# Optimization experiments

Measured on AMD Instinct MI355X. Metric: run time of the kernel, lower is better.

## Reference

```python
import jax, jax.numpy as jnp
import numpy as np

EPS = 1e-5
NEG_SLOPE = 0.01  # torch LeakyReLU default

def setup_inputs() -> dict:
    N, D, T, H = 4096, 64, 60, 128
    key = jax.random.key(0)
    ks = jax.random.split(key, 12)
    s_ih = 1.0 / np.sqrt(H)
    return {
        "x": jax.random.normal(ks[0], (N, D, T), dtype=jnp.float32),
        "bn1_gamma": jnp.ones((D,), jnp.float32),
        "bn1_beta": jnp.zeros((D,), jnp.float32),
        "W_ih": jax.random.uniform(ks[1], (4 * H, D), jnp.float32, -s_ih, s_ih),
        "W_hh": jax.random.uniform(ks[2], (4 * H, H), jnp.float32, -s_ih, s_ih),
        "b_ih": jax.random.uniform(ks[3], (4 * H,), jnp.float32, -s_ih, s_ih),
        "b_hh": jax.random.uniform(ks[4], (4 * H,), jnp.float32, -s_ih, s_ih),
        "bn2_gamma": jnp.ones((H,), jnp.float32),
        "bn2_beta": jnp.zeros((H,), jnp.float32),
        "W_t": jax.random.uniform(ks[5], (H, H), jnp.float32, -s_ih, s_ih),
        "b_t": jax.random.uniform(ks[6], (H,), jnp.float32, -s_ih, s_ih),
        "a": jax.random.normal(ks[7], (2 * H, 1), dtype=jnp.float32),
        "W_fc": jax.random.uniform(ks[8], (H, H), jnp.float32, -s_ih, s_ih),
        "b_fc": jax.random.uniform(ks[9], (H,), jnp.float32, -s_ih, s_ih),
        "W_out": jax.random.uniform(ks[10], (1, H), jnp.float32, -s_ih, s_ih),
        "b_out": jax.random.uniform(ks[11], (1,), jnp.float32, -s_ih, s_ih),
    }

def _leaky(z):
    return jnp.where(z >= 0, z, NEG_SLOPE * z)

def _lstm_last(x, W_ih, W_hh, b_ih, b_hh):
    # x: [N, T, D] -> last hidden state [N, H]
    N, T, D = x.shape
    H = W_hh.shape[1]
    # precompute input contributions for all timesteps: [T, N, 4H]
    xg = jnp.einsum('ntd,gd->tng', x, W_ih) + b_ih + b_hh
    h0 = jnp.zeros((N, H), x.dtype)
    c0 = jnp.zeros((N, H), x.dtype)
    def step(carry, g):
        h, c = carry
        gates = g + h @ W_hh.T
        i, f, gg, o = jnp.split(gates, 4, axis=-1)
        i = jax.nn.sigmoid(i)
        f = jax.nn.sigmoid(f)
        gg = jnp.tanh(gg)
        o = jax.nn.sigmoid(o)
        c = f * c + i * gg
        h = o * jnp.tanh(c)
        return (h, c), None
    (h, _), _ = jax.lax.scan(step, (h0, c0), xg)
    return h

def reference(x, bn1_gamma, bn1_beta, W_ih, W_hh, b_ih, b_hh,
              bn2_gamma, bn2_beta, W_t, b_t, a, W_fc, b_fc, W_out, b_out):
    # BatchNorm1d over channels of [N, D, T] (training-mode batch stats)
    m1 = x.mean(axis=(0, 2), keepdims=True)
    v1 = x.var(axis=(0, 2), keepdims=True)
    xn = (x - m1) * jax.lax.rsqrt(v1 + EPS)
    xn = xn * bn1_gamma[None, :, None] + bn1_beta[None, :, None]
    xs = jnp.transpose(xn, (0, 2, 1))  # [N, T, D]
    hidden = _lstm_last(xs, W_ih, W_hh, b_ih, b_hh)  # [N, H]
    # BatchNorm1d on [N, H]
    m2 = hidden.mean(axis=0, keepdims=True)
    v2 = hidden.var(axis=0, keepdims=True)
    hidden = (hidden - m2) * jax.lax.rsqrt(v2 + EPS) * bn2_gamma + bn2_beta
    # attention: scores[i,j] = a1.t[j] + a2.t[i]  (decomposed, no NxNx2H concat)
    H = hidden.shape[1]
    t = hidden @ W_t.T + b_t  # [N, H]
    s1 = t @ a[:H, 0]   # contribution of column node j
    s2 = t @ a[H:, 0]   # contribution of row node i
    scores = _leaky(s2[:, None] + s1[None, :])  # [N, N]
    att = jax.nn.softmax(scores, axis=1)
    h2 = att @ hidden + hidden
    h3 = _leaky(h2 @ W_fc.T + b_fc)
    out = jax.nn.sigmoid(h3 @ W_out.T + b_out)  # [N, 1]
    return out.squeeze(-1)
```

## Files before the change

### kernel.cpp

```cpp
#include <hip/hip_runtime.h>
#include <math.h>

constexpr int NN = 4096, DD = 64, TT = 60, HH = 128, GG = 512, KK = 192;

typedef _Float16 h8 __attribute__((ext_vector_type(8)));
typedef float f4 __attribute__((ext_vector_type(4)));

constexpr size_t XNT = 0;
constexpr size_t WFRG = (size_t)TT * NN * DD / 2;
constexpr size_t BSUM = WFRG + 98304 / 2;
constexpr size_t SC1 = BSUM + GG;
constexpr size_t SH1 = SC1 + DD;
constexpr size_t HID = SH1 + DD;
constexpr size_t HBN = HID + (size_t)NN * HH;
constexpr size_t SC2 = HBN + (size_t)NN * HH;
constexpr size_t SH2 = SC2 + HH;
constexpr size_t U1O = SH2 + HH;
constexpr size_t U2O = U1O + HH;
constexpr size_t CCO = U2O + HH;
constexpr size_t S1O = CCO + 4;
constexpr size_t S2O = S1O + NN;
constexpr size_t H2O = S2O + NN;
constexpr size_t SSUM = H2O + (size_t)NN * HH;
constexpr size_t SC16 = SSUM + 392;

__device__ __forceinline__ float fastrcp_(float x) { return __builtin_amdgcn_rcpf(x); }
__device__ __forceinline__ float sigmoidf_(float x) { return fastrcp_(1.f + __expf(-x)); }
__device__ __forceinline__ float tanhfast_(float x) { return 1.f - 2.f * fastrcp_(__expf(2.f * x) + 1.f); }
__device__ __forceinline__ float leakyf_(float z) { return fmaxf(z, 0.01f * z); }

__device__ __forceinline__ unsigned fenc_(float f) {
    unsigned b = __float_as_uint(f);
    return (b & 0x80000000u) ? ~b : (b | 0x80000000u);
}
__device__ __forceinline__ float fdec_(unsigned u) {
    return (u & 0x80000000u) ? __uint_as_float(u & 0x7fffffffu) : __uint_as_float(~u);
}

constexpr int TSTR = 264;

__global__ __launch_bounds__(256) void k_pre(const float* __restrict__ x,
                                             const float* __restrict__ Wih,
                                             const float* __restrict__ Whh,
                                             const float* __restrict__ Wt,
                                             const float* __restrict__ bt,
                                             const float* __restrict__ a,
                                             float* __restrict__ ws) {
    int b = blockIdx.x;
    int tid = threadIdx.x;
    if (b >= 1024) {
        if (b == 1408) {
            int k = tid;
            if (k < HH) {
                float u1 = 0.f, u2 = 0.f;
                for (int j = 0; j < HH; j++) {
                    float w = Wt[j * HH + k];
                    u1 = fmaf(w, a[j], u1);
                    u2 = fmaf(w, a[HH + j], u2);
                }
                ws[U1O + k] = u1;
                ws[U2O + k] = u2;
                if (k == 0) {
                    float c1 = 0.f, c2 = 0.f;
                    for (int j = 0; j < HH; j++) {
                        c1 = fmaf(bt[j], a[j], c1);
                        c2 = fmaf(bt[j], a[HH + j], c2);
                    }
                    ws[CCO] = c1;
                    ws[CCO + 1] = c2;
                    ((unsigned*)ws)[CCO + 2] = fenc_(-1e30f);
                }
            }
            return;
        }
        int o = (b - 1024) * 256 + tid;
        _Float16* wf = (_Float16*)(ws + WFRG);
        int j = o & 7;
        int lane = (o >> 3) & 63;
        int rest = o >> 9;
        int ks = rest % 6;
        int gw = rest / 6;
        int g = gw & 3, w = gw >> 2;
        int col = g * 128 + w * 16 + (lane & 15);
        int k = ks * 32 + (lane >> 4) * 8 + j;
        float v = (k < DD) ? Wih[col * DD + k] : Whh[col * HH + (k - DD)];
        wf[o] = (_Float16)v;
        return;
    }
    __shared__ _Float16 stg[TT * TSTR];
    __shared__ float rs[256], rss[256];
    const float4* xb = (const float4*)(x + (size_t)b * 15360);
#pragma unroll
    for (int q = 0; q < 15; q++) {
        int f = q * 256 + tid;
        float4 v = xb[f];
        int k = f / 15, t0 = (f - k * 15) * 4;
        stg[(t0 + 0) * TSTR + k] = (_Float16)v.x;
        stg[(t0 + 1) * TSTR + k] = (_Float16)v.y;
        stg[(t0 + 2) * TSTR + k] = (_Float16)v.z;
        stg[(t0 + 3) * TSTR + k] = (_Float16)v.w;
    }
    __syncthreads();
    {
        int k = tid;
        float s = 0.f, ss = 0.f;
#pragma unroll
        for (int t = 0; t < TT; t++) {
            float v = (float)stg[t * TSTR + k];
            s += v;
            ss = fmaf(v, v, ss);
        }
        rs[tid] = s; rss[tid] = ss;
    }
    __syncthreads();
    if (tid < 64) {
        float ts = rs[tid] + rs[64 + tid] + rs[128 + tid] + rs[192 + tid];
        float tss = rss[tid] + rss[64 + tid] + rss[128 + tid] + rss[192 + tid];
        float* pp = ws + H2O + (size_t)b * 128;
        pp[tid] = ts;
        pp[64 + tid] = tss;
    }
    _Float16* outp = (_Float16*)ws;
    int n0 = b * 4;
    for (int p = tid; p < 3840; p += 256) {
        int t = p >> 6, i = p & 63;
        *(uint2*)(outp + ((size_t)t * NN + n0) * DD + i * 4) =
            *(const uint2*)(stg + t * TSTR + i * 4);
    }
}

__global__ __launch_bounds__(256) void k_fin1(const float* __restrict__ g1,
                                              const float* __restrict__ b1,
                                              const float* __restrict__ Wih,
                                              const float* __restrict__ bih,
                                              const float* __restrict__ bhh,
                                              float* __restrict__ ws) {
    __shared__ float p2[8][128];
    __shared__ float scs[64], shs[64];
    int tid = threadIdx.x;
    for (int i = tid; i < 392; i += 256) ws[SSUM + i] = 0.f;
    {
        int rb = tid >> 5;
        int c0 = (tid & 31) * 4;
        const float* pb = ws + H2O + (size_t)rb * 128 * 128;
        float4 s4 = {0.f, 0.f, 0.f, 0.f};
        for (int bb = 0; bb < 128; bb++) {
            float4 v = *(const float4*)(pb + (size_t)bb * 128 + c0);
            s4.x += v.x; s4.y += v.y; s4.z += v.z; s4.w += v.w;
        }
        p2[rb][c0 + 0] = s4.x;
        p2[rb][c0 + 1] = s4.y;
        p2[rb][c0 + 2] = s4.z;
        p2[rb][c0 + 3] = s4.w;
    }
    __syncthreads();
    if (tid < 64) {
        float s_ = 0.f, ss_ = 0.f;
#pragma unroll
        for (int g = 0; g < 8; g++) {
            s_ += p2[g][tid];
            ss_ += p2[g][64 + tid];
        }
        float cnt = (float)(NN * TT);
        float m = s_ / cnt;
        float var = ss_ / cnt - m * m;
        float sc = g1[tid] * rsqrtf(var + 1e-5f);
        scs[tid] = sc;
        shs[tid] = b1[tid] - m * sc;
        ((_Float16*)(ws + SC16))[tid] = (_Float16)sc;
    }
    __syncthreads();
    for (int c = tid; c < GG; c += 256) {
        float bsum = bih[c] + bhh[c];
        const float4* wr = (const float4*)(Wih + c * 64);
#pragma unroll
        for (int q = 0; q < 16; q++) {
            float4 wv = wr[q];
            bsum = fmaf(wv.x, shs[q * 4], fmaf(wv.y, shs[q * 4 + 1],
                   fmaf(wv.z, shs[q * 4 + 2], fmaf(wv.w, shs[q * 4 + 3], bsum))));
        }
        ws[BSUM + c] = bsum;
    }
}

__global__ __launch_bounds__(512, 1) void k_lstm(float* __restrict__ ws) {
    int tid = threadIdx.x;
    int w = tid >> 6, lane = tid & 63;
    int quad = lane >> 4, m = lane & 15;
    int r0 = blockIdx.x * 16;
    __shared__ _Float16 hlds[2][16][136];
    const _Float16* wf = (const _Float16*)(ws + WFRG);

    h8 bw[4][6];
#pragma unroll
    for (int g = 0; g < 4; g++)
#pragma unroll
        for (int ks = 0; ks < 6; ks++)
            bw[g][ks] = *(const h8*)(wf + ((((w * 4 + g) * 6 + ks) * 64 + lane) * 8));

    f4 xbias[4];
#pragma unroll
    for (int g = 0; g < 4; g++) {
        float bv = ws[BSUM + g * 128 + w * 16 + m];
        xbias[g] = (f4){bv, bv, bv, bv};
    }

    const _Float16* sc16 = (const _Float16*)(ws + SC16);
    {
        h8 scv0 = *(const h8*)(sc16 + quad * 8);
        h8 scv1 = *(const h8*)(sc16 + 32 + quad * 8);
#pragma unroll
        for (int g = 0; g < 4; g++) { bw[g][0] *= scv0; bw[g][1] *= scv1; }
    }

    for (int p = tid; p < 2 * 16 * 136; p += 512) ((_Float16*)hlds)[p] = (_Float16)0.f;

    f4 cst = {};
    float hv[4];
    const _Float16* xb = (const _Float16*)ws + (size_t)(r0 + m) * DD + quad * 8;
    int col = w * 16 + m;
    __syncthreads();

    h8 ax0 = *(const h8*)xb;
    h8 ax1 = *(const h8*)(xb + 32);
    f4 xA[4], xB[4];
#pragma unroll
    for (int g = 0; g < 4; g++) xA[g] = __builtin_amdgcn_mfma_f32_16x16x32_f16(ax0, bw[g][0], xbias[g], 0, 0, 0);
#pragma unroll
    for (int g = 0; g < 4; g++) xA[g] = __builtin_amdgcn_mfma_f32_16x16x32_f16(ax1, bw[g][1], xA[g], 0, 0, 0);

    for (int t = 0; t < TT; t += 2) {
        {
            h8 ah[4];
            const _Float16* hb = &hlds[1][m][quad * 8];
#pragma unroll
            for (int ks = 0; ks < 4; ks++) ah[ks] = *(const h8*)(hb + ks * 32);
            const _Float16* xp = xb + (size_t)(t + 1) * NN * DD;
            h8 nx0 = *(const h8*)xp;
            h8 nx1 = *(const h8*)(xp + 32);
#pragma unroll
            for (int ks = 0; ks < 4; ks++)
#pragma unroll
                for (int g = 0; g < 4; g++)
                    xA[g] = __builtin_amdgcn_mfma_f32_16x16x32_f16(ah[ks], bw[g][ks + 2], xA[g], 0, 0, 0);
#pragma unroll
            for (int r = 0; r < 4; r++) {
                float ig = sigmoidf_(xA[0][r]);
                float fg = sigmoidf_(xA[1][r]);
                float gg = tanhfast_(xA[2][r]);
                float og = sigmoidf_(xA[3][r]);
                float c = fmaf(fg, cst[r], ig * gg);
                cst[r] = c;
                hv[r] = og * tanhfast_(c);
            }
            _Float16* wbuf = &hlds[0][0][0];
#pragma unroll
            for (int r = 0; r < 4; r++) wbuf[(quad * 4 + r) * 136 + col] = (_Float16)hv[r];
#pragma unroll
            for (int g = 0; g < 4; g++) xB[g] = __builtin_amdgcn_mfma_f32_16x16x32_f16(nx0, bw[g][0], xbias[g], 0, 0, 0);
#pragma unroll
            for (int g = 0; g < 4; g++) xB[g] = __builtin_amdgcn_mfma_f32_16x16x32_f16(nx1, bw[g][1], xB[g], 0, 0, 0);
            asm volatile("s_waitcnt lgkmcnt(0)\n\ts_barrier" ::: "memory");
        }
        {
            h8 ah[4];
            const _Float16* hb = &hlds[0][m][quad * 8];
#pragma unroll
            for (int ks = 0; ks < 4; ks++) ah[ks] = *(const h8*)(hb + ks * 32);
            h8 nx0 = {}, nx1 = {};
            if (t + 2 < TT) {
                const _Float16* xp = xb + (size_t)(t + 2) * NN * DD;
                nx0 = *(const h8*)xp;
                nx1 = *(const h8*)(xp + 32);
            }
#pragma unroll
            for (int ks = 0; ks < 4; ks++)
#pragma unroll
                for (int g = 0; g < 4; g++)
                    xB[g] = __builtin_amdgcn_mfma_f32_16x16x32_f16(ah[ks], bw[g][ks + 2], xB[g], 0, 0, 0);
#pragma unroll
            for (int r = 0; r < 4; r++) {
                float ig = sigmoidf_(xB[0][r]);
                float fg = sigmoidf_(xB[1][r]);
                float gg = tanhfast_(xB[2][r]);
                float og = sigmoidf_(xB[3][r]);
                float c = fmaf(fg, cst[r], ig * gg);
                cst[r] = c;
                hv[r] = og * tanhfast_(c);
            }
            _Float16* wbuf = &hlds[1][0][0];
#pragma unroll
            for (int r = 0; r < 4; r++) wbuf[(quad * 4 + r) * 136 + col] = (_Float16)hv[r];
#pragma unroll
            for (int g = 0; g < 4; g++) xA[g] = __builtin_amdgcn_mfma_f32_16x16x32_f16(nx0, bw[g][0], xbias[g], 0, 0, 0);
#pragma unroll
            for (int g = 0; g < 4; g++) xA[g] = __builtin_amdgcn_mfma_f32_16x16x32_f16(nx1, bw[g][1], xA[g], 0, 0, 0);
            asm volatile("s_waitcnt lgkmcnt(0)\n\ts_barrier" ::: "memory");
        }
    }
#pragma unroll
    for (int r = 0; r < 4; r++)
        ws[HID + (size_t)(r0 + quad * 4 + r) * HH + col] = hv[r];

    float s = hv[0] + hv[1] + hv[2] + hv[3];
    float ss = fmaf(hv[0], hv[0], fmaf(hv[1], hv[1], fmaf(hv[2], hv[2], hv[3] * hv[3])));
    s += __shfl_xor(s, 16, 64); s += __shfl_xor(s, 32, 64);
    ss += __shfl_xor(ss, 16, 64); ss += __shfl_xor(ss, 32, 64);
    if (quad == 0) {
        atomicAdd(&ws[SSUM + 132 + col], s);
        atomicAdd(&ws[SSUM + 260 + col], ss);
    }
}

__global__ void k_hbn(const float* __restrict__ g2,
                      const float* __restrict__ b2,
                      float* __restrict__ ws) {
    __shared__ float sc[HH], sh[HH], u1s[HH], u2s[HH];
    __shared__ _Float16 swz[4096];
    int tid = threadIdx.x;
    if (tid < HH) {
        float mm = ws[SSUM + 132 + tid] * (1.f / (float)NN);
        float var = ws[SSUM + 260 + tid] * (1.f / (float)NN) - mm * mm;
        float scv = g2[tid] * rsqrtf(var + 1e-5f);
        sc[tid] = scv;
        sh[tid] = b2[tid] - mm * scv;
        u1s[tid] = ws[U1O + tid]; u2s[tid] = ws[U2O + tid];
    }
    __syncthreads();
    int r = tid >> 3, l = tid & 7;
    int n = blockIdx.x * 32 + r;
    const float* hr = ws + HID + (size_t)n * HH;
    float* hb = ws + HBN + (size_t)n * HH;
    int lanehi = (r >> 3);
    int jj = r & 7;
    float d1 = 0.f, d2 = 0.f;
    int k0 = l * 16;
#pragma unroll
    for (int q4 = 0; q4 < 4; q4++) {
        float4 hv4 = *(const float4*)&hr[k0 + q4 * 4];
        float4 o;
#pragma unroll
        for (int c = 0; c < 4; c++) {
            int kk = k0 + q4 * 4 + c;
            float v = fmaf(((const float*)&hv4)[c], sc[kk], sh[kk]);
            ((float*)&o)[c] = v;
            swz[l * 512 + (lanehi * 16 + (kk & 15)) * 8 + jj] = (_Float16)v;
            d1 = fmaf(v, u1s[kk], d1);
            d2 = fmaf(v, u2s[kk], d2);
        }
        *(float4*)&hb[k0 + q4 * 4] = o;
    }
#pragma unroll
    for (int o = 1; o < 8; o <<= 1) { d1 += __shfl_xor(d1, o, 64); d2 += __shfl_xor(d2, o, 64); }
    if (l == 0) {
        float s1 = d1 + ws[CCO];
        ws[S1O + n] = s1;
        ws[S2O + n] = d2 + ws[CCO + 1];
        atomicMax((unsigned*)ws + CCO + 2, fenc_(s1));
    }
    __syncthreads();
    _Float16* dst = (_Float16*)ws + (size_t)blockIdx.x * 4096;
    for (int p = tid; p < 512; p += 256)
        *(h8*)(dst + p * 8) = *(const h8*)(swz + p * 8);
}

__global__ __launch_bounds__(512, 1) void k_attfc(const float* __restrict__ Wfc,
                                                  const float* __restrict__ bfc,
                                                  const float* __restrict__ Wout,
                                                  const float* __restrict__ bout,
                                                  float* __restrict__ ws,
                                                  float* __restrict__ out) {
    __shared__ float ls1[NN];
    __shared__ float red[4][16][132];
    __shared__ float psr[4][16];
    __shared__ float h2s[16][132];
    int tid = threadIdx.x;
    int w = tid >> 6, lane = tid & 63;
    int quad = lane >> 4, m = lane & 15;
    int whalf = w >> 2, jsplit = w & 3;
    int n0 = blockIdx.x * 16;
    for (int i = tid; i < NN; i += 512) ls1[i] = ws[S1O + i];
    __syncthreads();
    float s1max = fdec_(((unsigned*)ws)[CCO + 2]);
    float s2n = ws[S2O + n0 + m];
    float mi = leakyf_(s2n + s1max);
    const _Float16* hbsw = (const _Float16*)ws;
    f4 acc[4] = {};
    float psum = 0.f;
    for (int jt0 = 0; jt0 < 32; jt0++) {
        int jt = jsplit * 32 + jt0;
        const float* sp = &ls1[jt * 32 + quad * 8];
        h8 ap;
        float ps = 0.f;
#pragma unroll
        for (int jj = 0; jj < 8; jj++) {
            float z = s2n + sp[jj];
            float p = __expf(leakyf_(z) - mi);
            ps += p;
            ap[jj] = (_Float16)p;
        }
        psum += ps;
#pragma unroll
        for (int hgi = 0; hgi < 4; hgi++) {
            int hg = whalf * 4 + hgi;
            h8 bb = *(const h8*)(hbsw + ((size_t)(jt * 8 + hg) * 64 + lane) * 8);
            acc[hgi] = __builtin_amdgcn_mfma_f32_16x16x32_f16(ap, bb, acc[hgi], 0, 0, 0);
        }
    }
    psum += __shfl_xor(psum, 16, 64);
    psum += __shfl_xor(psum, 32, 64);
    if (whalf == 0 && lane < 16) psr[jsplit][lane] = psum;
#pragma unroll
    for (int hgi = 0; hgi < 4; hgi++) {
        int h = (whalf * 4 + hgi) * 16 + m;
#pragma unroll
        for (int r = 0; r < 4; r++)
            red[jsplit][quad * 4 + r][h] = acc[hgi][r];
    }
    __syncthreads();
    if (tid < 16) {
        float pt = psr[0][tid] + psr[1][tid] + psr[2][tid] + psr[3][tid];
        psr[0][tid] = fastrcp_(pt);
    }
    __syncthreads();
#pragma unroll
    for (int cc = 0; cc < 4; cc++) {
        int c = cc * 512 + tid;
        int row = c >> 7, h = c & 127;
        float v = red[0][row][h] + red[1][row][h] + red[2][row][h] + red[3][row][h];
        h2s[row][h] = fmaf(v, psr[0][row], ws[HBN + (size_t)(n0 + row) * HH + h]);
    }
    __syncthreads();
    int row = tid >> 5, jj = tid & 31;
    float po = 0.f;
#pragma unroll
    for (int q = 0; q < 4; q++) {
        int j = q * 32 + jj;
        const float4* wr = (const float4*)(Wfc + (size_t)j * HH);
        float a = 0.f;
#pragma unroll 8
        for (int kq = 0; kq < 32; kq++) {
            float4 wv = wr[kq];
            float4 hv = *(const float4*)&h2s[row][kq * 4];
            a = fmaf(wv.x, hv.x, fmaf(wv.y, hv.y, fmaf(wv.z, hv.z, fmaf(wv.w, hv.w, a))));
        }
        po = fmaf(leakyf_(a + bfc[j]), Wout[j], po);
    }
#pragma unroll
    for (int o = 1; o < 32; o <<= 1) po += __shfl_xor(po, o, 64);
    if (jj == 0) out[n0 + row] = fastrcp_(1.f + __expf(-(po + bout[0])));
}

extern "C" void kernel_launch(void* const* d_in, const int* in_sizes, int n_in,
                              void* d_out, int out_size, void* d_ws, size_t ws_size,
                              hipStream_t stream) {
    const float* x = (const float*)d_in[0];
    const float* bn1_g = (const float*)d_in[1];
    const float* bn1_b = (const float*)d_in[2];
    const float* W_ih = (const float*)d_in[3];
    const float* W_hh = (const float*)d_in[4];
    const float* b_ih = (const float*)d_in[5];
    const float* b_hh = (const float*)d_in[6];
    const float* bn2_g = (const float*)d_in[7];
    const float* bn2_b = (const float*)d_in[8];
    const float* W_t = (const float*)d_in[9];
    const float* b_t = (const float*)d_in[10];
    const float* a = (const float*)d_in[11];
    const float* W_fc = (const float*)d_in[12];
    const float* b_fc = (const float*)d_in[13];
    const float* W_out = (const float*)d_in[14];
    const float* b_out = (const float*)d_in[15];
    float* ws = (float*)d_ws;
    float* out = (float*)d_out;

    k_pre<<<1409, 256, 0, stream>>>(x, W_ih, W_hh, W_t, b_t, a, ws);
    k_fin1<<<1, 256, 0, stream>>>(bn1_g, bn1_b, W_ih, b_ih, b_hh, ws);
    k_lstm<<<NN / 16, 512, 0, stream>>>(ws);
    k_hbn<<<NN / 32, 256, 0, stream>>>(bn2_g, bn2_b, ws);
    k_attfc<<<NN / 16, 512, 0, stream>>>(W_fc, b_fc, W_out, b_out, ws, out);
}
```

Before: 265.4 us.

## Widen small kernels, pad staging stride, double-buffer attention MFMA loop

The single-block BN1 finalize kernel now runs with 1024 threads, which shortens each thread's serial reduction over the partial sums. The hidden-BN kernel uses 512 threads, each handling 8 features instead of 16. In the attention kernel the loop is software-pipelined: the next tile's B fragments are loaded and its probabilities computed before the current tile's MFMAs issue. The k_pre LDS staging stride changes from 264 to 266 to avoid bank conflicts. Together these aim to cut serial latency in the small kernels and hide load latency in attention, at the cost of higher register pressure.

Measured after the change: 284.3 us. 1.07x slower.

```diff
diff --git a/kernel.cpp b/kernel.cpp
--- a/kernel.cpp
+++ b/kernel.cpp
@@ -37,7 +37,7 @@
     return (u & 0x80000000u) ? __uint_as_float(u & 0x7fffffffu) : __uint_as_float(~u);
 }
 
-constexpr int TSTR = 264;
+constexpr int TSTR = 266;
 
 __global__ __launch_bounds__(256) void k_pre(const float* __restrict__ x,
                                              const float* __restrict__ Wih,
@@ -129,22 +129,22 @@
     }
 }
 
-__global__ __launch_bounds__(256) void k_fin1(const float* __restrict__ g1,
-                                              const float* __restrict__ b1,
-                                              const float* __restrict__ Wih,
-                                              const float* __restrict__ bih,
-                                              const float* __restrict__ bhh,
-                                              float* __restrict__ ws) {
-    __shared__ float p2[8][128];
+__global__ __launch_bounds__(1024) void k_fin1(const float* __restrict__ g1,
+                                               const float* __restrict__ b1,
+                                               const float* __restrict__ Wih,
+                                               const float* __restrict__ bih,
+                                               const float* __restrict__ bhh,
+                                               float* __restrict__ ws) {
+    __shared__ float p2[32][128];
     __shared__ float scs[64], shs[64];
     int tid = threadIdx.x;
-    for (int i = tid; i < 392; i += 256) ws[SSUM + i] = 0.f;
+    if (tid < 392) ws[SSUM + tid] = 0.f;
     {
         int rb = tid >> 5;
         int c0 = (tid & 31) * 4;
-        const float* pb = ws + H2O + (size_t)rb * 128 * 128;
+        const float* pb = ws + H2O + (size_t)rb * 32 * 128;
         float4 s4 = {0.f, 0.f, 0.f, 0.f};
-        for (int bb = 0; bb < 128; bb++) {
+        for (int bb = 0; bb < 32; bb++) {
             float4 v = *(const float4*)(pb + (size_t)bb * 128 + c0);
             s4.x += v.x; s4.y += v.y; s4.z += v.z; s4.w += v.w;
         }
@@ -157,7 +157,7 @@
     if (tid < 64) {
         float s_ = 0.f, ss_ = 0.f;
 #pragma unroll
-        for (int g = 0; g < 8; g++) {
+        for (int g = 0; g < 32; g++) {
             s_ += p2[g][tid];
             ss_ += p2[g][64 + tid];
         }
@@ -170,14 +170,18 @@
         ((_Float16*)(ws + SC16))[tid] = (_Float16)sc;
     }
     __syncthreads();
-    for (int c = tid; c < GG; c += 256) {
+    if (tid < GG) {
+        int c = tid;
         float bsum = bih[c] + bhh[c];
         const float4* wr = (const float4*)(Wih + c * 64);
+        float4 sh4[16];
+#pragma unroll
+        for (int q = 0; q < 16; q++) sh4[q] = *(const float4*)&shs[q * 4];
 #pragma unroll
         for (int q = 0; q < 16; q++) {
             float4 wv = wr[q];
-            bsum = fmaf(wv.x, shs[q * 4], fmaf(wv.y, shs[q * 4 + 1],
-                   fmaf(wv.z, shs[q * 4 + 2], fmaf(wv.w, shs[q * 4 + 3], bsum))));
+            bsum = fmaf(wv.x, sh4[q].x, fmaf(wv.y, sh4[q].y,
+                   fmaf(wv.z, sh4[q].z, fmaf(wv.w, sh4[q].w, bsum))));
         }
         ws[BSUM + c] = bsum;
     }
@@ -312,9 +316,9 @@
     }
 }
 
-__global__ void k_hbn(const float* __restrict__ g2,
-                      const float* __restrict__ b2,
-                      float* __restrict__ ws) {
+__global__ __launch_bounds__(512) void k_hbn(const float* __restrict__ g2,
+                                             const float* __restrict__ b2,
+                                             float* __restrict__ ws) {
     __shared__ float sc[HH], sh[HH], u1s[HH], u2s[HH];
     __shared__ _Float16 swz[4096];
     int tid = threadIdx.x;
@@ -327,16 +331,14 @@
         u1s[tid] = ws[U1O + tid]; u2s[tid] = ws[U2O + tid];
     }
     __syncthreads();
-    int r = tid >> 3, l = tid & 7;
+    int r = tid >> 4, l = tid & 15;
     int n = blockIdx.x * 32 + r;
     const float* hr = ws + HID + (size_t)n * HH;
     float* hb = ws + HBN + (size_t)n * HH;
-    int lanehi = (r >> 3);
-    int jj = r & 7;
     float d1 = 0.f, d2 = 0.f;
-    int k0 = l * 16;
-#pragma unroll
-    for (int q4 = 0; q4 < 4; q4++) {
+    int k0 = l * 8;
+#pragma unroll
+    for (int q4 = 0; q4 < 2; q4++) {
         float4 hv4 = *(const float4*)&hr[k0 + q4 * 4];
         float4 o;
 #pragma unroll
@@ -344,14 +346,14 @@
             int kk = k0 + q4 * 4 + c;
             float v = fmaf(((const float*)&hv4)[c], sc[kk], sh[kk]);
             ((float*)&o)[c] = v;
-            swz[l * 512 + (lanehi * 16 + (kk & 15)) * 8 + jj] = (_Float16)v;
+            swz[(kk >> 4) * 512 + ((r >> 3) * 16 + (kk & 15)) * 8 + (r & 7)] = (_Float16)v;
             d1 = fmaf(v, u1s[kk], d1);
             d2 = fmaf(v, u2s[kk], d2);
         }
         *(float4*)&hb[k0 + q4 * 4] = o;
     }
 #pragma unroll
-    for (int o = 1; o < 8; o <<= 1) { d1 += __shfl_xor(d1, o, 64); d2 += __shfl_xor(d2, o, 64); }
+    for (int o = 1; o < 16; o <<= 1) { d1 += __shfl_xor(d1, o, 64); d2 += __shfl_xor(d2, o, 64); }
     if (l == 0) {
         float s1 = d1 + ws[CCO];
         ws[S1O + n] = s1;
@@ -360,8 +362,7 @@
     }
     __syncthreads();
     _Float16* dst = (_Float16*)ws + (size_t)blockIdx.x * 4096;
-    for (int p = tid; p < 512; p += 256)
-        *(h8*)(dst + p * 8) = *(const h8*)(swz + p * 8);
+    *(h8*)(dst + tid * 8) = *(const h8*)(swz + tid * 8);
 }
 
 __global__ __launch_bounds__(512, 1) void k_attfc(const float* __restrict__ Wfc,
@@ -387,26 +388,51 @@
     const _Float16* hbsw = (const _Float16*)ws;
     f4 acc[4] = {};
     float psum = 0.f;
-    for (int jt0 = 0; jt0 < 32; jt0++) {
-        int jt = jsplit * 32 + jt0;
-        const float* sp = &ls1[jt * 32 + quad * 8];
-        h8 ap;
-        float ps = 0.f;
-#pragma unroll
-        for (int jj = 0; jj < 8; jj++) {
-            float z = s2n + sp[jj];
-            float p = __expf(leakyf_(z) - mi);
-            ps += p;
-            ap[jj] = (_Float16)p;
-        }
-        psum += ps;
-#pragma unroll
-        for (int hgi = 0; hgi < 4; hgi++) {
-            int hg = whalf * 4 + hgi;
-            h8 bb = *(const h8*)(hbsw + ((size_t)(jt * 8 + hg) * 64 + lane) * 8);
-            acc[hgi] = __builtin_amdgcn_mfma_f32_16x16x32_f16(ap, bb, acc[hgi], 0, 0, 0);
-        }
-    }
+
+#define AP_COMPUTE(JT, APV, PSV)                                        \
+    {                                                                   \
+        const float* sp_ = &ls1[(JT) * 32 + quad * 8];                  \
+        PSV = 0.f;                                                      \
+        _Pragma("unroll")                                               \
+        for (int jj = 0; jj < 8; jj++) {                                \
+            float z = s2n + sp_[jj];                                    \
+            float p = __expf(leakyf_(z) - mi);                          \
+            PSV += p;                                                   \
+            APV[jj] = (_Float16)p;                                      \
+        }                                                               \
+    }
+#define BB_LOAD(JT, BBV)                                                \
+    {                                                                   \
+        _Pragma("unroll")                                               \
+        for (int hgi = 0; hgi < 4; hgi++)                               \
+            BBV[hgi] = *(const h8*)(hbsw +                              \
+                ((size_t)((JT) * 8 + whalf * 4 + hgi) * 64 + lane) * 8);\
+    }
+
+    h8 apA, apB, bbA[4], bbB[4];
+    float psA, psB;
+    int jt0base = jsplit * 32;
+    AP_COMPUTE(jt0base, apA, psA);
+    BB_LOAD(jt0base, bbA);
+    for (int jt0 = 0; jt0 < 32; jt0 += 2) {
+        BB_LOAD(jt0base + jt0 + 1, bbB);
+        AP_COMPUTE(jt0base + jt0 + 1, apB, psB);
+        psum += psA;
+#pragma unroll
+        for (int hgi = 0; hgi < 4; hgi++)
+            acc[hgi] = __builtin_amdgcn_mfma_f32_16x16x32_f16(apA, bbA[hgi], acc[hgi], 0, 0, 0);
+        if (jt0 + 2 < 32) {
+            BB_LOAD(jt0base + jt0 + 2, bbA);
+            AP_COMPUTE(jt0base + jt0 + 2, apA, psA);
+        }
+        psum += psB;
+#pragma unroll
+        for (int hgi = 0; hgi < 4; hgi++)
+            acc[hgi] = __builtin_amdgcn_mfma_f32_16x16x32_f16(apB, bbB[hgi], acc[hgi], 0, 0, 0);
+    }
+#undef AP_COMPUTE
+#undef BB_LOAD
+
     psum += __shfl_xor(psum, 16, 64);
     psum += __shfl_xor(psum, 32, 64);
     if (whalf == 0 && lane < 16) psr[jsplit][lane] = psum;
@@ -474,8 +500,8 @@
     float* out = (float*)d_out;
 
     k_pre<<<1409, 256, 0, stream>>>(x, W_ih, W_hh, W_t, b_t, a, ws);
-    k_fin1<<<1, 256, 0, stream>>>(bn1_g, bn1_b, W_ih, b_ih, b_hh, ws);
+    k_fin1<<<1, 1024, 0, stream>>>(bn1_g, bn1_b, W_ih, b_ih, b_hh, ws);
     k_lstm<<<NN / 16, 512, 0, stream>>>(ws);
-    k_hbn<<<NN / 32, 256, 0, stream>>>(bn2_g, bn2_b, ws);
+    k_hbn<<<NN / 32, 512, 0, stream>>>(bn2_g, bn2_b, ws);
     k_attfc<<<NN / 16, 512, 0, stream>>>(W_fc, b_fc, W_out, b_out, ws, out);
 }
```
